# Performance work log

Hardware: AMD Instinct MI355X
Metric: run time of the kernel (lower is better)

## Reference

```python
import jax, jax.numpy as jnp
import numpy as np
import math

VOCAB = 256
EMBED = 1024
HEADS = 16
MAX_SEQ = 1024
B, S = 4, 1024
EPS = 1e-5


def setup_inputs() -> dict:
    key = jax.random.key(0)
    ks = jax.random.split(key, 10)
    x = jax.random.randint(ks[0], (B, S), 0, VOCAB)
    token_embedding = jax.random.normal(ks[1], (VOCAB, EMBED), dtype=jnp.float32)
    # positional phase buffer: pos * (1/10000**(dim/E)) * pi
    pos = jnp.arange(MAX_SEQ, dtype=jnp.float32)[:, None]
    dim = jnp.arange(EMBED, dtype=jnp.float32)[None, :]
    freq = 1.0 / (10000.0 ** (dim / EMBED))
    pos_phase = pos * freq * math.pi  # [MAX_SEQ, EMBED]
    hd = EMBED // HEADS
    q_rot = jax.random.uniform(ks[2], (HEADS, hd), minval=-math.pi, maxval=math.pi)
    k_rot = jax.random.uniform(ks[3], (HEADS, hd), minval=-math.pi, maxval=math.pi)
    v_rot = jax.random.uniform(ks[4], (HEADS, hd), minval=-math.pi, maxval=math.pi)
    # orthogonal-ish init for ff_real via QR
    a = jax.random.normal(ks[5], (EMBED, EMBED), dtype=jnp.float32)
    ff_real, _ = jnp.linalg.qr(a)
    ff_imag = jax.random.uniform(ks[6], (EMBED, EMBED), minval=-0.01, maxval=0.01)
    lim = 1.0 / math.sqrt(EMBED)
    ro_real_w = jax.random.uniform(ks[7], (VOCAB, EMBED), minval=-lim, maxval=lim)
    ro_real_b = jnp.zeros((VOCAB,), dtype=jnp.float32)
    ro_imag_w = jax.random.uniform(ks[8], (VOCAB, EMBED), minval=-lim, maxval=lim)
    ro_imag_b = jnp.zeros((VOCAB,), dtype=jnp.float32)
    return {
        "x": x,
        "token_embedding": token_embedding,
        "pos_phase": pos_phase,
        "q_rot": q_rot,
        "k_rot": k_rot,
        "v_rot": v_rot,
        "ff_real": ff_real,
        "ff_imag": ff_imag,
        "ro_real_w": ro_real_w,
        "ro_real_b": ro_real_b,
        "ro_imag_w": ro_imag_w,
        "ro_imag_b": ro_imag_b,
    }


def complex_norm(z):
    mag = jnp.abs(z)
    mean_mag = jnp.mean(mag, axis=-1, keepdims=True)
    std_mag = jnp.std(mag, axis=-1, keepdims=True, ddof=1)  # torch std is unbiased
    norm_mag = (mag - mean_mag) / (std_mag + EPS)
    scale = jnp.tanh(norm_mag) / (mag + EPS)
    return z * scale.astype(jnp.complex64)


def reference(x, token_embedding, pos_phase, q_rot, k_rot, v_rot,
              ff_real, ff_imag, ro_real_w, ro_real_b, ro_imag_w, ro_imag_b):
    b, s = x.shape
    h, hd = q_rot.shape
    mag = jnp.tanh(token_embedding[x])                       # [B,S,E]
    state = mag.astype(jnp.complex64) * jnp.exp(1j * pos_phase[:s].astype(jnp.complex64))[None]
    sh = state.reshape(b, s, h, hd)                          # [B,S,H,hd]
    q = sh * jnp.exp(1j * q_rot.astype(jnp.complex64))
    k = sh * jnp.exp(1j * k_rot.astype(jnp.complex64))
    v = sh * jnp.exp(1j * v_rot.astype(jnp.complex64))
    # complex QK^H interference -> take real part as logits
    interference = jnp.einsum('bqhd,bkhd->bhqk', q, jnp.conj(k))
    attn_logits = interference.real / math.sqrt(hd)
    causal = jnp.tril(jnp.ones((s, s), dtype=bool))
    attn_logits = jnp.where(causal[None, None], attn_logits, -jnp.inf)
    attn_weights = jax.nn.softmax(attn_logits * 8.0, axis=-1)  # [B,H,S,S]
    attn_out = jnp.einsum('bhqk,bkhd->bqhd', attn_weights.astype(jnp.complex64), v)
    attn_out = attn_out.reshape(b, s, h * hd)
    state = state + attn_out
    ff = ff_real.astype(jnp.complex64) + 1j * ff_imag.astype(jnp.complex64)
    state = state @ ff
    state = complex_norm(state)
    return state.real @ ro_real_w.T + ro_real_b + state.imag @ ro_imag_w.T + ro_imag_b
```

## Files before the change

### kernel.cpp

```cpp
#include <hip/hip_runtime.h>
#include <math.h>

#define B_ 4
#define S_ 1024
#define E_ 1024
#define H_ 16
#define V_ 256

typedef _Float16 h8 __attribute__((ext_vector_type(8)));
typedef _Float16 h4 __attribute__((ext_vector_type(4)));
typedef __fp16 f16x2 __attribute__((ext_vector_type(2)));
typedef int i2 __attribute__((ext_vector_type(2)));
typedef float f4x __attribute__((ext_vector_type(4)));

__device__ __forceinline__ void gload16(const void* g, void* l) {
  __builtin_amdgcn_global_load_lds((const __attribute__((address_space(1))) void*)g,
                                   (__attribute__((address_space(3))) void*)l, 16, 0, 0);
}

#define MFMA32F16(a, b, c) __builtin_amdgcn_mfma_f32_16x16x32_f16(a, b, c, 0, 0, 0)

#if defined(__has_builtin)
#if __has_builtin(__builtin_amdgcn_mfma_f32_16x16x16f16)
#define MFMA16F16(a, b, c) __builtin_amdgcn_mfma_f32_16x16x16f16(a, b, c, 0, 0, 0)
#endif
#endif
#ifndef MFMA16F16
__device__ __forceinline__ f4x mfma16f16_asm(h4 a, h4 b, f4x c) {
  asm volatile("v_mfma_f32_16x16x16_f16 %0, %1, %2, %0" : "+v"(c) : "v"(a), "v"(b));
  return c;
}
#define MFMA16F16(a, b, c) mfma16f16_asm(a, b, c)
#endif

__device__ __forceinline__ float fast_tanh(float x) {
  return 1.0f - 2.0f / (__expf(2.0f * x) + 1.0f);
}
__device__ __forceinline__ float fast_exp2(float x) {
  float r;
  asm("v_exp_f32 %0, %1" : "=v"(r) : "v"(x));
  return r;
}

__global__ void rot_kernel(const float* __restrict__ qr, const float* __restrict__ kr,
                           const float* __restrict__ vr, float* __restrict__ tabs) {
  int i = blockIdx.x * blockDim.x + threadIdx.x;
  if (i >= 4 * 1024) return;
  int which = i >> 10;
  int j = i & 1023;
  if (which < 3) {
    const float* src = which == 0 ? qr : (which == 1 ? kr : vr);
    float s, c;
    sincosf(src[j], &s, &c);
    tabs[which * 2048 + j] = c;
    tabs[which * 2048 + 1024 + j] = s;
  } else {
    float g = 0.5f * exp2f(-(float)j * (13.287712379549449f / 1024.0f));
    tabs[6144 + j] = g;
  }
}

__global__ __launch_bounds__(256) void embed_qkv_kernel(
    const int* __restrict__ x, const float* __restrict__ te,
    const float* __restrict__ tabs,
    unsigned short* __restrict__ srh, unsigned short* __restrict__ sih,
    unsigned short* __restrict__ Kd, unsigned short* __restrict__ Vd) {
  __shared__ unsigned short Kl2[4096];
  __shared__ unsigned short Vl2[4096];
  const int kt2 = blockIdx.x;
  const int bh = blockIdx.y;
  const int b = bh >> 4, h = bh & 15;
  const int tid = threadIdx.x;
  const float* qc = tabs + h * 64;
  const float* qs = tabs + 1024 + h * 64;
  const float* kc = tabs + 2048 + h * 64;
  const float* ks = tabs + 3072 + h * 64;
  const float* gt = tabs + 6144 + h * 64;
  #pragma unroll
  for (int p = 0; p < 8; ++p) {
    int id = p * 256 + tid;
    int sl = id >> 6;
    int dd = id & 63;
    int s = kt2 * 32 + sl;
    int e = h * 64 + dd;
    int tok = x[b * 1024 + s];
    float mm = fast_tanh(te[tok * 1024 + e]);
    float rev = (float)s * gt[dd];
    rev = rev - floorf(rev);
    float sn, cs;
    asm("v_sin_f32 %0, %1" : "=v"(sn) : "v"(rev));
    asm("v_cos_f32 %0, %1" : "=v"(cs) : "v"(rev));
    float re = mm * cs, im = mm * sn;
    size_t g = ((size_t)(b * 1024 + s)) * 1024 + e;
    *(_Float16*)&srh[g] = (_Float16)re;
    *(_Float16*)&sih[g] = (_Float16)im;
    float cq = qc[dd], sq = qs[dd], ck = kc[dd], sk = ks[dd];
    float cd = cq * ck + sq * sk;
    float sd = sq * ck - cq * sk;
    float kr = re * cd + im * sd;
    float ki = im * cd - re * sd;
    int t = sl >> 4, key = sl & 15;
    int c0 = dd, c1 = 64 + dd;
    #define KOFF(c) (t * 2048 + ((((c) >> 5) * 4 + (((c) >> 3) & 3)) * 16 + key) * 8 + ((c) & 7))
    *(_Float16*)&Kl2[KOFF(c0)] = (_Float16)kr;
    *(_Float16*)&Kl2[KOFF(c1)] = (_Float16)ki;
    #undef KOFF
    int kgk = key >> 2, jk = key & 3;
    #define VOFF(d) (t * 2048 + ((((d) >> 4) * 4 + kgk) * 16 + ((d) & 15)) * 4 + jk)
    *(_Float16*)&Vl2[VOFF(dd)] = (_Float16)re;
    *(_Float16*)&Vl2[VOFF(64 + dd)] = (_Float16)im;
    #undef VOFF
  }
  __syncthreads();
  unsigned short* kdst = Kd + ((size_t)(bh * 64 + kt2 * 2)) * 2048;
  unsigned short* vdst = Vd + ((size_t)(bh * 64 + kt2 * 2)) * 2048;
  #pragma unroll
  for (int p = 0; p < 2; ++p) {
    int c = p * 256 + tid;
    ((int4*)kdst)[c] = ((const int4*)Kl2)[c];
    ((int4*)vdst)[c] = ((const int4*)Vl2)[c];
  }
}

__global__ __launch_bounds__(256, 4) void attn_mfma_kernel(
    const unsigned short* __restrict__ srh, const unsigned short* __restrict__ sih,
    const unsigned short* __restrict__ Kd, const unsigned short* __restrict__ Vd,
    const float* __restrict__ tabs,
    unsigned short* __restrict__ Af) {
  __shared__ __align__(16) unsigned short Klds[2][4096];
  __shared__ __align__(16) unsigned short Vlds[2][4096];
  const int flat = blockIdx.x;
  const int low = flat & 7, rest = flat >> 3;
  const int a = rest >> 3;
  const int bh = ((rest & 7) << 3) | low;
  const int b = bh >> 4, h = bh & 15;
  const int tid = threadIdx.x, lane = tid & 63, wid = tid >> 6;
  const int cl = lane & 15, kg = lane >> 4;
  const int atile = (wid >> 1) ? (31 - a) : a;
  const int qw0 = atile * 32 + (wid & 1) * 16;

  h8 qf[4];
  {
    int q = qw0 + cl;
    const unsigned short* srow = srh + ((size_t)(b * 1024 + q)) * 1024 + h * 64;
    const unsigned short* irow = sih + ((size_t)(b * 1024 + q)) * 1024 + h * 64;
    #pragma unroll
    for (int ksx = 0; ksx < 4; ++ksx) {
      int f0 = ksx * 32 + kg * 8;
      qf[ksx] = (f0 < 64) ? *(const h8*)(srow + f0) : *(const h8*)(irow + (f0 - 64));
      qf[ksx] *= (_Float16)1.4426950408889634f;
    }
  }

  f4x acc[8] = {};
  float m_ = -1e30f, l_ = 0.f;
  const int np = 32 - a;
  const int wqmax = qw0 + 15;
  const int qcol = qw0 + cl;

  const unsigned short* kstream = Kd + ((size_t)(bh * 64)) * 2048;
  const unsigned short* vstream = Vd + ((size_t)(bh * 64)) * 2048;

  #define STAGE_PAIR(buf, P)                                                    \
    {                                                                           \
      const unsigned short* kb = kstream + (size_t)(P) * 4096;                  \
      const unsigned short* vb = vstream + (size_t)(P) * 4096;                  \
      _Pragma("unroll")                                                         \
      for (int r = 0; r < 2; ++r) {                                             \
        int off = r * 256 + wid * 64;                                           \
        gload16(kb + (size_t)(off + lane) * 8, &Klds[buf][off * 8]);            \
        gload16(vb + (size_t)(off + lane) * 8, &Vlds[buf][off * 8]);            \
      }                                                                         \
    }

  STAGE_PAIR(0, 0)
  __syncthreads();

  for (int p = 0; p < np; ++p) {
    const int cur = p & 1;
    if (p + 1 < np) STAGE_PAIR(cur ^ 1, p + 1)
    const int k0a = p * 32;
    if (k0a <= wqmax) {
      __builtin_amdgcn_s_setprio(1);
      f4x sca = {}, scb = {};
      #pragma unroll
      for (int ksx = 0; ksx < 4; ++ksx) {
        h8 ka = *(const h8*)&Klds[cur][ksx * 512 + lane * 8];
        sca = MFMA32F16(ka, qf[ksx], sca);
      }
      #pragma unroll
      for (int ksx = 0; ksx < 4; ++ksx) {
        h8 kb = *(const h8*)&Klds[cur][2048 + ksx * 512 + lane * 8];
        scb = MFMA32F16(kb, qf[ksx], scb);
      }
      __builtin_amdgcn_s_setprio(0);
      if (k0a + 31 > qw0) {
        #pragma unroll
        for (int r = 0; r < 4; ++r) {
          if (k0a + kg * 4 + r > qcol)      sca[r] = -1e30f;
          if (k0a + 16 + kg * 4 + r > qcol) scb[r] = -1e30f;
        }
      }
      float mA = fmaxf(fmaxf(sca[0], sca[1]), sca[2]);
      float mB = fmaxf(fmaxf(sca[3], scb[0]), scb[1]);
      float mC = fmaxf(fmaxf(scb[2], scb[3]), mA);
      float mx = fmaxf(mB, mC);
      mx = fmaxf(mx, __shfl_xor(mx, 16, 64));
      mx = fmaxf(mx, __shfl_xor(mx, 32, 64));
      if (!__all(mx <= m_ + 11.5416f)) {
        float mn = fmaxf(m_, mx);
        float corr = fast_exp2(m_ - mn);
        #pragma unroll
        for (int mt = 0; mt < 8; ++mt) acc[mt] *= corr;
        l_ *= corr;
        m_ = mn;
      }
      float pa0 = fast_exp2(sca[0] - m_), pa1 = fast_exp2(sca[1] - m_);
      float pa2 = fast_exp2(sca[2] - m_), pa3 = fast_exp2(sca[3] - m_);
      float pb0 = fast_exp2(scb[0] - m_), pb1 = fast_exp2(scb[1] - m_);
      float pb2 = fast_exp2(scb[2] - m_), pb3 = fast_exp2(scb[3] - m_);
      l_ += ((pa0 + pa1) + (pa2 + pa3)) + ((pb0 + pb1) + (pb2 + pb3));
      f16x2 a01 = __builtin_amdgcn_cvt_pkrtz(pa0, pa1);
      f16x2 a23 = __builtin_amdgcn_cvt_pkrtz(pa2, pa3);
      f16x2 b01 = __builtin_amdgcn_cvt_pkrtz(pb0, pb1);
      f16x2 b23 = __builtin_amdgcn_cvt_pkrtz(pb2, pb3);
      i2 ta, tb;
      ta[0] = __builtin_bit_cast(int, a01); ta[1] = __builtin_bit_cast(int, a23);
      tb[0] = __builtin_bit_cast(int, b01); tb[1] = __builtin_bit_cast(int, b23);
      h4 pba = __builtin_bit_cast(h4, ta);
      h4 pbb = __builtin_bit_cast(h4, tb);
      __builtin_amdgcn_s_setprio(1);
      #pragma unroll
      for (int mt = 0; mt < 8; ++mt) {
        h4 va = *(const h4*)&Vlds[cur][mt * 256 + lane * 4];
        acc[mt] = MFMA16F16(va, pba, acc[mt]);
      }
      #pragma unroll
      for (int mt = 0; mt < 8; ++mt) {
        h4 vb = *(const h4*)&Vlds[cur][2048 + mt * 256 + lane * 4];
        acc[mt] = MFMA16F16(vb, pbb, acc[mt]);
      }
      __builtin_amdgcn_s_setprio(0);
    }
    __syncthreads();
  }
  #undef STAGE_PAIR
  {
    l_ += __shfl_xor(l_, 16, 64);
    l_ += __shfl_xor(l_, 32, 64);
    float linv = 1.0f / l_;
    int q = qw0 + cl;
    size_t mrow = (size_t)(b * 1024 + q);
    size_t obase = mrow * 1024 + h * 64;
    size_t abase = mrow * 2048 + h * 64;
    #pragma unroll
    for (int mt = 0; mt < 4; ++mt) {
      int d0 = mt * 16 + kg * 4;
      h4 s_r = *(const h4*)&srh[obase + d0];
      h4 s_i = *(const h4*)&sih[obase + d0];
      h4 hr, hi;
      #pragma unroll
      for (int r = 0; r < 4; ++r) {
        int d = d0 + r;
        float orv = acc[mt][r] * linv;
        float oiv = acc[mt + 4][r] * linv;
        float c = tabs[4096 + h * 64 + d], s = tabs[5120 + h * 64 + d];
        hr[r] = (_Float16)(orv * c - oiv * s + (float)s_r[r]);
        hi[r] = (_Float16)(orv * s + oiv * c + (float)s_i[r]);
      }
      *(h4*)&Af[abase + d0]        = hr;
      *(h4*)&Af[abase + 1024 + d0] = hi;
    }
  }
}

__global__ void split_b_kernel(const float* __restrict__ fr, const float* __restrict__ fi,
                               unsigned short* __restrict__ Bt) {
  __shared__ float tile[32][33];
  const int k0 = blockIdx.x * 32, n0 = blockIdx.y * 32;
  const int tid = threadIdx.x;
  #pragma unroll
  for (int p = 0; p < 4; ++p) {
    int e = p * 256 + tid;
    int kk = e >> 5, nn = e & 31;
    int k = k0 + kk, n = n0 + nn;
    float v;
    if (n < 1024) v = (k < 1024) ? fr[(size_t)k * 1024 + n] : -fi[(size_t)(k - 1024) * 1024 + n];
    else          v = (k < 1024) ? fi[(size_t)k * 1024 + (n - 1024)]
                                 : fr[(size_t)(k - 1024) * 1024 + (n - 1024)];
    tile[kk][nn] = v;
  }
  __syncthreads();
  #pragma unroll
  for (int p = 0; p < 4; ++p) {
    int e = p * 256 + tid;
    int nn = e >> 5, kk = e & 31;
    *(_Float16*)&Bt[(size_t)(n0 + nn) * 2048 + (k0 + kk)] = (_Float16)tile[kk][nn];
  }
}

__global__ void split_w_kernel(const float* __restrict__ wr, const float* __restrict__ wi,
                               unsigned short* __restrict__ Wt) {
  int idx = blockIdx.x * 256 + threadIdx.x;
  int v = idx >> 9;
  int k4 = (idx & 511) * 4;
  float4 a = (k4 < 1024) ? *(const float4*)&wr[(size_t)v * 1024 + k4]
                         : *(const float4*)&wi[(size_t)v * 1024 + k4 - 1024];
  h4 h;
  h[0] = (_Float16)a.x; h[1] = (_Float16)a.y;
  h[2] = (_Float16)a.z; h[3] = (_Float16)a.w;
  *(h4*)&Wt[(size_t)v * 2048 + k4] = h;
}

__global__ __launch_bounds__(256, 2) void gemm_ff(
    const unsigned short* __restrict__ A,
    const unsigned short* __restrict__ Bt,
    float* __restrict__ pr0, float* __restrict__ pi0,
    float* __restrict__ pr1, float* __restrict__ pi1) {
  __shared__ short As[256 * 64];
  __shared__ short Bs[128 * 64];
  const int tid = threadIdx.x;
  const int lane = tid & 63, wid = tid >> 6;
  const int l = blockIdx.x + (blockIdx.y << 4);
  const int xcd = l & 7, j = l >> 3;
  const int m0 = ((xcd << 1) + (j & 1)) << 8;
  const int n0 = (j >> 1) << 7;
  const int z = blockIdx.z;
  const int wr = wid >> 1, wc = wid & 1;
  const int cl = lane & 15, rg = lane >> 4;

  f4x acc[8][4] = {};

  for (int kt = z * 16; kt < z * 16 + 16; ++kt) {
    const int k0 = kt * 64;
    #pragma unroll
    for (int it = 0; it < 8; ++it) {
      int c = wid * 512 + it * 64 + lane;
      gload16(A + (size_t)(m0 + (c >> 3)) * 2048 + k0 + (c & 7) * 8,
              As + (wid * 512 + it * 64) * 8);
    }
    #pragma unroll
    for (int it = 0; it < 4; ++it) {
      int c = wid * 256 + it * 64 + lane;
      gload16(Bt + (size_t)(n0 + (c >> 3)) * 2048 + k0 + (c & 7) * 8,
              Bs + (wid * 256 + it * 64) * 8);
    }
    __syncthreads();
    #pragma unroll
    for (int ks = 0; ks < 2; ++ks) {
      h8 a[8], b[4];
      #pragma unroll
      for (int ms = 0; ms < 8; ++ms)
        a[ms] = *(const h8*)&As[(wr * 128 + ms * 16 + cl) * 64 + ks * 32 + rg * 8];
      #pragma unroll
      for (int ns = 0; ns < 4; ++ns)
        b[ns] = *(const h8*)&Bs[(wc * 64 + ns * 16 + cl) * 64 + ks * 32 + rg * 8];
      #pragma unroll
      for (int ms = 0; ms < 8; ++ms)
        #pragma unroll
        for (int ns = 0; ns < 4; ++ns)
          acc[ms][ns] = MFMA32F16(a[ms], b[ns], acc[ms][ns]);
    }
    __syncthreads();
  }

  const int colbase = n0 + wc * 64;
  float* o_r = z ? pr1 : pr0;
  float* o_i = z ? pi1 : pi0;
  float* dst = (colbase < 1024) ? o_r : o_i;
  const int cb = colbase & 1023;
  #pragma unroll
  for (int ms = 0; ms < 8; ++ms)
    #pragma unroll
    for (int r2 = 0; r2 < 4; ++r2) {
      const int grow = m0 + wr * 128 + ms * 16 + rg * 4 + r2;
      #pragma unroll
      for (int ns = 0; ns < 4; ++ns)
        dst[(size_t)grow * 1024 + cb + ns * 16 + cl] = acc[ms][ns][r2];
    }
}

__global__ __launch_bounds__(256, 4) void gemm_ro(
    const unsigned short* __restrict__ Z,
    const unsigned short* __restrict__ Wt,
    float* __restrict__ part) {
  __shared__ short As[128 * 64];
  __shared__ short Bs[128 * 64];
  const int tid = threadIdx.x;
  const int lane = tid & 63, wid = tid >> 6;
  const int l = blockIdx.x + (blockIdx.y << 5);
  const int xcd = l & 7, j = l >> 3;
  const int m0 = ((xcd << 2) + (j & 3)) << 7;
  const int n0 = (j >> 2) << 7;
  const int z = blockIdx.z;
  const int wr = wid >> 1, wc = wid & 1;
  const int cl = lane & 15, rg = lane >> 4;

  f4x acc[4][4] = {};
  const int cbase = wid * 256;

  for (int kt = z * 8; kt < z * 8 + 8; ++kt) {
    const int k0 = kt * 64;
    #pragma unroll
    for (int it = 0; it < 4; ++it) {
      int c = cbase + it * 64 + lane;
      gload16(Z + (size_t)(m0 + (c >> 3)) * 2048 + k0 + (c & 7) * 8,
              As + (cbase + it * 64) * 8);
      gload16(Wt + (size_t)(n0 + (c >> 3)) * 2048 + k0 + (c & 7) * 8,
              Bs + (cbase + it * 64) * 8);
    }
    __syncthreads();
    #pragma unroll
    for (int ks = 0; ks < 2; ++ks) {
      h8 a[4], b[4];
      #pragma unroll
      for (int ms = 0; ms < 4; ++ms)
        a[ms] = *(const h8*)&As[(wr * 64 + ms * 16 + cl) * 64 + ks * 32 + rg * 8];
      #pragma unroll
      for (int ns = 0; ns < 4; ++ns)
        b[ns] = *(const h8*)&Bs[(wc * 64 + ns * 16 + cl) * 64 + ks * 32 + rg * 8];
      #pragma unroll
      for (int ms = 0; ms < 4; ++ms)
        #pragma unroll
        for (int ns = 0; ns < 4; ++ns)
          acc[ms][ns] = MFMA32F16(a[ms], b[ns], acc[ms][ns]);
    }
    __syncthreads();
  }

  float* dst = part + (size_t)z * 4096 * 256;
  const int colbase = n0 + wc * 64;
  #pragma unroll
  for (int ms = 0; ms < 4; ++ms)
    #pragma unroll
    for (int r2 = 0; r2 < 4; ++r2) {
      const int grow = m0 + wr * 64 + ms * 16 + rg * 4 + r2;
      #pragma unroll
      for (int ns = 0; ns < 4; ++ns)
        dst[(size_t)grow * 256 + colbase + ns * 16 + cl] = acc[ms][ns][r2];
    }
}

__global__ __launch_bounds__(256) void norm_split_kernel(
    const float* __restrict__ pr0, const float* __restrict__ pi0,
    const float* __restrict__ pr1, const float* __restrict__ pi1,
    unsigned short* __restrict__ Z) {
  const int row = blockIdx.x, tid = threadIdx.x;
  const int base = row * E_ + tid * 4;
  float4 r0 = *(const float4*)&pr0[base];
  float4 r1 = *(const float4*)&pr1[base];
  float4 i0 = *(const float4*)&pi0[base];
  float4 i1 = *(const float4*)&pi1[base];
  float4 zr = make_float4(r0.x + r1.x, r0.y + r1.y, r0.z + r1.z, r0.w + r1.w);
  float4 zi = make_float4(i0.x + i1.x, i0.y + i1.y, i0.z + i1.z, i0.w + i1.w);
  float mg[4];
  mg[0] = sqrtf(zr.x * zr.x + zi.x * zi.x);
  mg[1] = sqrtf(zr.y * zr.y + zi.y * zi.y);
  mg[2] = sqrtf(zr.z * zr.z + zi.z * zi.z);
  mg[3] = sqrtf(zr.w * zr.w + zi.w * zi.w);
  float s1 = mg[0] + mg[1] + mg[2] + mg[3];
  float s2 = mg[0]*mg[0] + mg[1]*mg[1] + mg[2]*mg[2] + mg[3]*mg[3];
  #pragma unroll
  for (int off = 1; off < 64; off <<= 1) {
    s1 += __shfl_xor(s1, off, 64);
    s2 += __shfl_xor(s2, off, 64);
  }
  __shared__ float ws1[4], ws2[4];
  if ((tid & 63) == 0) { ws1[tid >> 6] = s1; ws2[tid >> 6] = s2; }
  __syncthreads();
  s1 = ws1[0] + ws1[1] + ws1[2] + ws1[3];
  s2 = ws2[0] + ws2[1] + ws2[2] + ws2[3];
  float mean = s1 * (1.0f / 1024.0f);
  float var = (s2 - 1024.0f * mean * mean) * (1.0f / 1023.0f);
  var = fmaxf(var, 0.0f);
  float inv_sd = 1.0f / (sqrtf(var) + 1e-5f);
  float sc[4];
  #pragma unroll
  for (int t = 0; t < 4; ++t)
    sc[t] = tanhf((mg[t] - mean) * inv_sd) / (mg[t] + 1e-5f);
  h4 hr, hi;
  hr[0] = (_Float16)(zr.x * sc[0]); hr[1] = (_Float16)(zr.y * sc[1]);
  hr[2] = (_Float16)(zr.z * sc[2]); hr[3] = (_Float16)(zr.w * sc[3]);
  hi[0] = (_Float16)(zi.x * sc[0]); hi[1] = (_Float16)(zi.y * sc[1]);
  hi[2] = (_Float16)(zi.z * sc[2]); hi[3] = (_Float16)(zi.w * sc[3]);
  const size_t zb = (size_t)row * 2048 + tid * 4;
  *(h4*)&Z[zb]        = hr;
  *(h4*)&Z[zb + 1024] = hi;
}

__global__ void reduce_bias_kernel(const float* __restrict__ part,
                                   const float* __restrict__ rb,
                                   const float* __restrict__ ib,
                                   float* __restrict__ out) {
  int i4 = (blockIdx.x * 256 + threadIdx.x) * 4;
  int col = i4 & 255;
  float4 s = *(const float4*)&part[i4];
  #pragma unroll
  for (int z = 1; z < 4; ++z) {
    float4 v = *(const float4*)&part[(size_t)z * 1048576 + i4];
    s.x += v.x; s.y += v.y; s.z += v.z; s.w += v.w;
  }
  s.x += rb[col + 0] + ib[col + 0];
  s.y += rb[col + 1] + ib[col + 1];
  s.z += rb[col + 2] + ib[col + 2];
  s.w += rb[col + 3] + ib[col + 3];
  *(float4*)&out[i4] = s;
}

extern "C" void kernel_launch(void* const* d_in, const int* in_sizes, int n_in,
                              void* d_out, int out_size, void* d_ws, size_t ws_size,
                              hipStream_t stream) {
  const int*   x    = (const int*)d_in[0];
  const float* te   = (const float*)d_in[1];
  const float* qr   = (const float*)d_in[3];
  const float* kr   = (const float*)d_in[4];
  const float* vr   = (const float*)d_in[5];
  const float* ffr  = (const float*)d_in[6];
  const float* ffi  = (const float*)d_in[7];
  const float* rorw = (const float*)d_in[8];
  const float* rorb = (const float*)d_in[9];
  const float* roiw = (const float*)d_in[10];
  const float* roib = (const float*)d_in[11];
  float* out = (float*)d_out;

  char* W = (char*)d_ws;
  const size_t MiB = 1 << 20;
  unsigned short* srh = (unsigned short*)W;
  unsigned short* sih = (unsigned short*)(W + 16 * MiB);
  unsigned short* Af = (unsigned short*)(W + 32 * MiB);
  unsigned short* Kd = (unsigned short*)(W + 48 * MiB);
  unsigned short* Vd = (unsigned short*)(W + 64 * MiB);
  unsigned short* Bt = (unsigned short*)(W + 48 * MiB);
  unsigned short* Wt = (unsigned short*)(W + 56 * MiB);
  float* tabs = (float*)(W + 96 * MiB);
  float* pr0 = (float*)W;
  float* pi0 = (float*)(W + 16 * MiB);
  float* pr1 = (float*)(W + 64 * MiB);
  float* pi1 = (float*)(W + 80 * MiB);
  unsigned short* Zhl = Af;
  float* ro_part = (float*)(W + 64 * MiB);

  rot_kernel<<<16, 256, 0, stream>>>(qr, kr, vr, tabs);
  embed_qkv_kernel<<<dim3(32, 64), 256, 0, stream>>>(x, te, tabs, srh, sih, Kd, Vd);
  attn_mfma_kernel<<<1024, 256, 0, stream>>>(srh, sih, Kd, Vd, tabs, Af);
  split_b_kernel<<<dim3(64, 64), 256, 0, stream>>>(ffr, ffi, Bt);
  split_w_kernel<<<512, 256, 0, stream>>>(rorw, roiw, Wt);
  gemm_ff<<<dim3(16, 16, 2), 256, 0, stream>>>(Af, Bt, pr0, pi0, pr1, pi1);
  norm_split_kernel<<<B_ * S_, 256, 0, stream>>>(pr0, pi0, pr1, pi1, Zhl);
  gemm_ro<<<dim3(32, 2, 4), 256, 0, stream>>>(Zhl, Wt, ro_part);
  reduce_bias_kernel<<<1024, 256, 0, stream>>>(ro_part, rorb, roib, out);
}
```

Baseline: 144.2 us.

## Replace split-K ff GEMM with 128x128 tiles, 8 waves, no partial sums

The feed-forward GEMM previously used 256x128 tiles with a split-K of 2, writing two fp32 partial buffers that the norm kernel then summed. It now uses 128x128 tiles with 512 threads (8 waves, each computing 64x32) over the full K range, writing the result once. This removes the extra partial-sum writes and reads and gives smaller per-wave accumulators for higher occupancy. In exchange, each tile does less compute per byte loaded and each block runs a longer serial K loop.

```diff
diff --git a/kernel.cpp b/kernel.cpp
--- a/kernel.cpp
+++ b/kernel.cpp
@@ -312,70 +312,63 @@
   *(h4*)&Wt[(size_t)v * 2048 + k4] = h;
 }
 
-__global__ __launch_bounds__(256, 2) void gemm_ff(
+__global__ __launch_bounds__(512, 4) void gemm_ff(
     const unsigned short* __restrict__ A,
     const unsigned short* __restrict__ Bt,
-    float* __restrict__ pr0, float* __restrict__ pi0,
-    float* __restrict__ pr1, float* __restrict__ pi1) {
-  __shared__ short As[256 * 64];
+    float* __restrict__ pr, float* __restrict__ pi) {
+  __shared__ short As[128 * 64];
   __shared__ short Bs[128 * 64];
   const int tid = threadIdx.x;
   const int lane = tid & 63, wid = tid >> 6;
-  const int l = blockIdx.x + (blockIdx.y << 4);
+  const int l = blockIdx.x + (blockIdx.y << 5);
   const int xcd = l & 7, j = l >> 3;
-  const int m0 = ((xcd << 1) + (j & 1)) << 8;
-  const int n0 = (j >> 1) << 7;
-  const int z = blockIdx.z;
-  const int wr = wid >> 1, wc = wid & 1;
+  const int m0 = ((xcd << 2) + (j & 3)) << 7;
+  const int n0 = (j >> 2) << 7;
+  const int wm = wid & 1, wn = wid >> 1;
   const int cl = lane & 15, rg = lane >> 4;
-
-  f4x acc[8][4] = {};
-
-  for (int kt = z * 16; kt < z * 16 + 16; ++kt) {
+  const int cb4 = wid * 128;
+
+  f4x acc[4][2] = {};
+
+  for (int kt = 0; kt < 32; ++kt) {
     const int k0 = kt * 64;
     #pragma unroll
-    for (int it = 0; it < 8; ++it) {
-      int c = wid * 512 + it * 64 + lane;
+    for (int it = 0; it < 2; ++it) {
+      int c = cb4 + it * 64 + lane;
       gload16(A + (size_t)(m0 + (c >> 3)) * 2048 + k0 + (c & 7) * 8,
-              As + (wid * 512 + it * 64) * 8);
-    }
-    #pragma unroll
-    for (int it = 0; it < 4; ++it) {
-      int c = wid * 256 + it * 64 + lane;
+              As + (cb4 + it * 64) * 8);
       gload16(Bt + (size_t)(n0 + (c >> 3)) * 2048 + k0 + (c & 7) * 8,
-              Bs + (wid * 256 + it * 64) * 8);
+              Bs + (cb4 + it * 64) * 8);
     }
     __syncthreads();
     #pragma unroll
     for (int ks = 0; ks < 2; ++ks) {
-      h8 a[8], b[4];
-      #pragma unroll
-      for (int ms = 0; ms < 8; ++ms)
-        a[ms] = *(const h8*)&As[(wr * 128 + ms * 16 + cl) * 64 + ks * 32 + rg * 8];
-      #pragma unroll
-      for (int ns = 0; ns < 4; ++ns)
-        b[ns] = *(const h8*)&Bs[(wc * 64 + ns * 16 + cl) * 64 + ks * 32 + rg * 8];
-      #pragma unroll
-      for (int ms = 0; ms < 8; ++ms)
+      h8 a[4], b[2];
+      #pragma unroll
+      for (int ms = 0; ms < 4; ++ms)
+        a[ms] = *(const h8*)&As[(wm * 64 + ms * 16 + cl) * 64 + ks * 32 + rg * 8];
+      #pragma unroll
+      for (int ns = 0; ns < 2; ++ns)
+        b[ns] = *(const h8*)&Bs[(wn * 32 + ns * 16 + cl) * 64 + ks * 32 + rg * 8];
+      #pragma unroll
+      for (int ms = 0; ms < 4; ++ms)
         #pragma unroll
-        for (int ns = 0; ns < 4; ++ns)
+        for (int ns = 0; ns < 2; ++ns)
           acc[ms][ns] = MFMA32F16(a[ms], b[ns], acc[ms][ns]);
     }
     __syncthreads();
   }
 
-  const int colbase = n0 + wc * 64;
-  float* o_r = z ? pr1 : pr0;
-  float* o_i = z ? pi1 : pi0;
-  float* dst = (colbase < 1024) ? o_r : o_i;
+  const int colbase = n0 + wn * 32;
+  float* dst = (colbase < 1024) ? pr : pi;
   const int cb = colbase & 1023;
   #pragma unroll
-  for (int ms = 0; ms < 8; ++ms)
+  for (int ms = 0; ms < 4; ++ms)
     #pragma unroll
     for (int r2 = 0; r2 < 4; ++r2) {
-      const int grow = m0 + wr * 128 + ms * 16 + rg * 4 + r2;
-      #pragma unroll
-      for (int ns = 0; ns < 4; ++ns)
+      const int grow = m0 + wm * 64 + ms * 16 + rg * 4 + r2;
+      #pragma unroll
+      for (int ns = 0; ns < 2; ++ns)
         dst[(size_t)grow * 1024 + cb + ns * 16 + cl] = acc[ms][ns][r2];
     }
 }
@@ -442,17 +435,12 @@
 }
 
 __global__ __launch_bounds__(256) void norm_split_kernel(
-    const float* __restrict__ pr0, const float* __restrict__ pi0,
-    const float* __restrict__ pr1, const float* __restrict__ pi1,
+    const float* __restrict__ pr, const float* __restrict__ pi,
     unsigned short* __restrict__ Z) {
   const int row = blockIdx.x, tid = threadIdx.x;
   const int base = row * E_ + tid * 4;
-  float4 r0 = *(const float4*)&pr0[base];
-  float4 r1 = *(const float4*)&pr1[base];
-  float4 i0 = *(const float4*)&pi0[base];
-  float4 i1 = *(const float4*)&pi1[base];
-  float4 zr = make_float4(r0.x + r1.x, r0.y + r1.y, r0.z + r1.z, r0.w + r1.w);
-  float4 zi = make_float4(i0.x + i1.x, i0.y + i1.y, i0.z + i1.z, i0.w + i1.w);
+  float4 zr = *(const float4*)&pr[base];
+  float4 zi = *(const float4*)&pi[base];
   float mg[4];
   mg[0] = sqrtf(zr.x * zr.x + zi.x * zi.x);
   mg[1] = sqrtf(zr.y * zr.y + zi.y * zi.y);
@@ -533,10 +521,8 @@
   unsigned short* Bt = (unsigned short*)(W + 48 * MiB);
   unsigned short* Wt = (unsigned short*)(W + 56 * MiB);
   float* tabs = (float*)(W + 96 * MiB);
-  float* pr0 = (float*)W;
-  float* pi0 = (float*)(W + 16 * MiB);
-  float* pr1 = (float*)(W + 64 * MiB);
-  float* pi1 = (float*)(W + 80 * MiB);
+  float* pr = (float*)W;
+  float* pi = (float*)(W + 16 * MiB);
   unsigned short* Zhl = Af;
   float* ro_part = (float*)(W + 64 * MiB);
 
@@ -545,8 +531,8 @@
   attn_mfma_kernel<<<1024, 256, 0, stream>>>(srh, sih, Kd, Vd, tabs, Af);
   split_b_kernel<<<dim3(64, 64), 256, 0, stream>>>(ffr, ffi, Bt);
   split_w_kernel<<<512, 256, 0, stream>>>(rorw, roiw, Wt);
-  gemm_ff<<<dim3(16, 16, 2), 256, 0, stream>>>(Af, Bt, pr0, pi0, pr1, pi1);
-  norm_split_kernel<<<B_ * S_, 256, 0, stream>>>(pr0, pi0, pr1, pi1, Zhl);
+  gemm_ff<<<dim3(32, 16), 512, 0, stream>>>(Af, Bt, pr, pi);
+  norm_split_kernel<<<B_ * S_, 256, 0, stream>>>(pr, pi, Zhl);
   gemm_ro<<<dim3(32, 2, 4), 256, 0, stream>>>(Zhl, Wt, ro_part);
   reduce_bias_kernel<<<1024, 256, 0, stream>>>(ro_part, rorb, roib, out);
 }
```

Result: slower. 153.7 us (+6.6%).

## Double-buffer gemm_ff with 256x256 tiles, swizzled LDS and 512 threads

Applied to the files above, without the earlier changes.

Rewrites the FF complex GEMM main loop to use two LDS buffers, prefetching the k-tile two steps ahead with global_load_lds and using vmcnt waits and raw barriers instead of full syncthreads. Block tile grows from 256x128 to 256x256 with 8 waves per block, and the LDS layout is XOR-swizzled to avoid bank conflicts on the fragment reads. The intent is to overlap global loads with MFMA work and cut LDS conflicts. In exchange it uses 128KB of LDS per block, which limits occupancy to one block per CU, and launches half as many blocks (256).

```diff
diff --git a/kernel.cpp b/kernel.cpp
--- a/kernel.cpp
+++ b/kernel.cpp
@@ -312,57 +312,85 @@
   *(h4*)&Wt[(size_t)v * 2048 + k4] = h;
 }
 
-__global__ __launch_bounds__(256, 2) void gemm_ff(
+__global__ __launch_bounds__(512, 2) void gemm_ff(
     const unsigned short* __restrict__ A,
     const unsigned short* __restrict__ Bt,
     float* __restrict__ pr0, float* __restrict__ pi0,
     float* __restrict__ pr1, float* __restrict__ pi1) {
-  __shared__ short As[256 * 64];
-  __shared__ short Bs[128 * 64];
+  __shared__ short As[2][16384];
+  __shared__ short Bs[2][16384];
   const int tid = threadIdx.x;
   const int lane = tid & 63, wid = tid >> 6;
   const int l = blockIdx.x + (blockIdx.y << 4);
   const int xcd = l & 7, j = l >> 3;
   const int m0 = ((xcd << 1) + (j & 1)) << 8;
-  const int n0 = (j >> 1) << 7;
+  const int n0 = (j >> 1) << 8;
   const int z = blockIdx.z;
-  const int wr = wid >> 1, wc = wid & 1;
+  const int wr = wid >> 2, wc = wid & 3;
   const int cl = lane & 15, rg = lane >> 4;
+  const int swz = (cl & 7) * 8;
+  const int kbase = z * 1024;
+  const int NT = 16;
 
   f4x acc[8][4] = {};
 
-  for (int kt = z * 16; kt < z * 16 + 16; ++kt) {
-    const int k0 = kt * 64;
-    #pragma unroll
-    for (int it = 0; it < 8; ++it) {
-      int c = wid * 512 + it * 64 + lane;
-      gload16(A + (size_t)(m0 + (c >> 3)) * 2048 + k0 + (c & 7) * 8,
-              As + (wid * 512 + it * 64) * 8);
-    }
-    #pragma unroll
-    for (int it = 0; it < 4; ++it) {
-      int c = wid * 256 + it * 64 + lane;
-      gload16(Bt + (size_t)(n0 + (c >> 3)) * 2048 + k0 + (c & 7) * 8,
-              Bs + (wid * 256 + it * 64) * 8);
-    }
-    __syncthreads();
+  #define FF_STAGE(bf, kt)                                                      \
+    {                                                                           \
+      const int k0s = kbase + (kt) * 64;                                        \
+      _Pragma("unroll")                                                         \
+      for (int it = 0; it < 4; ++it) {                                          \
+        int c = it * 512 + wid * 64 + lane;                                     \
+        int row = c >> 3;                                                       \
+        int colL = ((c & 7) ^ (row & 7)) * 8;                                   \
+        gload16(A + (size_t)(m0 + row) * 2048 + k0s + colL,                     \
+                &As[bf][(it * 512 + wid * 64) * 8]);                            \
+      }                                                                         \
+      _Pragma("unroll")                                                         \
+      for (int it = 0; it < 4; ++it) {                                          \
+        int c = it * 512 + wid * 64 + lane;                                     \
+        int row = c >> 3;                                                       \
+        int colL = ((c & 7) ^ (row & 7)) * 8;                                   \
+        gload16(Bt + (size_t)(n0 + row) * 2048 + k0s + colL,                    \
+                &Bs[bf][(it * 512 + wid * 64) * 8]);                            \
+      }                                                                         \
+    }
+
+  FF_STAGE(0, 0)
+  FF_STAGE(1, 1)
+  asm volatile("s_waitcnt vmcnt(8)" ::: "memory");
+  __builtin_amdgcn_s_barrier();
+
+  for (int t = 0; t < NT; ++t) {
+    const int bf = t & 1;
+    __builtin_amdgcn_s_setprio(1);
     #pragma unroll
     for (int ks = 0; ks < 2; ++ks) {
+      const int col = (ks * 32 + rg * 8) ^ swz;
       h8 a[8], b[4];
       #pragma unroll
       for (int ms = 0; ms < 8; ++ms)
-        a[ms] = *(const h8*)&As[(wr * 128 + ms * 16 + cl) * 64 + ks * 32 + rg * 8];
+        a[ms] = *(const h8*)&As[bf][(wr * 128 + ms * 16 + cl) * 64 + col];
       #pragma unroll
       for (int ns = 0; ns < 4; ++ns)
-        b[ns] = *(const h8*)&Bs[(wc * 64 + ns * 16 + cl) * 64 + ks * 32 + rg * 8];
+        b[ns] = *(const h8*)&Bs[bf][(wc * 64 + ns * 16 + cl) * 64 + col];
       #pragma unroll
       for (int ms = 0; ms < 8; ++ms)
         #pragma unroll
         for (int ns = 0; ns < 4; ++ns)
           acc[ms][ns] = MFMA32F16(a[ms], b[ns], acc[ms][ns]);
     }
-    __syncthreads();
-  }
+    __builtin_amdgcn_s_setprio(0);
+    asm volatile("s_waitcnt lgkmcnt(0)" ::: "memory");
+    __builtin_amdgcn_s_barrier();
+    if (t + 2 < NT) {
+      FF_STAGE(bf, t + 2)
+      asm volatile("s_waitcnt vmcnt(8)" ::: "memory");
+    } else if (t + 1 < NT) {
+      asm volatile("s_waitcnt vmcnt(0)" ::: "memory");
+    }
+    __builtin_amdgcn_s_barrier();
+  }
+  #undef FF_STAGE
 
   const int colbase = n0 + wc * 64;
   float* o_r = z ? pr1 : pr0;
@@ -545,7 +573,7 @@
   attn_mfma_kernel<<<1024, 256, 0, stream>>>(srh, sih, Kd, Vd, tabs, Af);
   split_b_kernel<<<dim3(64, 64), 256, 0, stream>>>(ffr, ffi, Bt);
   split_w_kernel<<<512, 256, 0, stream>>>(rorw, roiw, Wt);
-  gemm_ff<<<dim3(16, 16, 2), 256, 0, stream>>>(Af, Bt, pr0, pi0, pr1, pi1);
+  gemm_ff<<<dim3(16, 8, 2), 512, 0, stream>>>(Af, Bt, pr0, pi0, pr1, pi1);
   norm_split_kernel<<<B_ * S_, 256, 0, stream>>>(pr0, pi0, pr1, pi1, Zhl);
   gemm_ro<<<dim3(32, 2, 4), 256, 0, stream>>>(Zhl, Wt, ro_part);
   reduce_bias_kernel<<<1024, 256, 0, stream>>>(ro_part, rorb, roib, out);
```

New measurement: 146.3 us. About the same (+1.4%).
